# Kernel tuning notes

Measured on AMD Instinct MI355X. Metric: run time of the kernel, lower is better.

The kernel has to match this reference:

```python
import jax, jax.numpy as jnp
import numpy as np

N, E, R, B, H, C = 50000, 1600000, 50, 30, 16, 4


def setup_inputs() -> dict:
    key = jax.random.key(0)
    ks = jax.random.split(key, 12)
    edge_index = jax.random.randint(ks[0], (2, E), 0, N, dtype=jnp.int64)
    edge_type = jax.random.randint(ks[1], (E,), 0, R, dtype=jnp.int64)
    edge_norm = jax.random.uniform(ks[2], (E,), dtype=jnp.float32)
    s = 0.1
    basis1 = jax.random.normal(ks[3], (B, N, H), dtype=jnp.float32) * s
    comp1 = jax.random.normal(ks[4], (R, B), dtype=jnp.float32) * s
    root1 = jax.random.normal(ks[5], (N, H), dtype=jnp.float32) * s
    bias1 = jnp.zeros((H,), dtype=jnp.float32)
    basis2 = jax.random.normal(ks[6], (B, H, C), dtype=jnp.float32) * s
    comp2 = jax.random.normal(ks[7], (R, B), dtype=jnp.float32) * s
    root2 = jax.random.normal(ks[8], (H, C), dtype=jnp.float32) * s
    bias2 = jnp.zeros((C,), dtype=jnp.float32)
    return {
        "edge_index": edge_index, "edge_type": edge_type, "edge_norm": edge_norm,
        "basis1": basis1, "comp1": comp1, "root1": root1, "bias1": bias1,
        "basis2": basis2, "comp2": comp2, "root2": root2, "bias2": bias2,
    }


def _scatter_mean(msg, dst, n):
    # mean aggregation over destination nodes (PyG RGCNConv aggr='mean')
    summed = jnp.zeros((n, msg.shape[1]), dtype=msg.dtype).at[dst].add(msg)
    cnt = jnp.zeros((n,), dtype=msg.dtype).at[dst].add(1.0)
    return summed / jnp.maximum(cnt, 1.0)[:, None]


def reference(edge_index, edge_type, edge_norm, basis1, comp1, root1, bias1,
              basis2, comp2, root2, bias2):
    # edge_norm is accepted but unused, matching the original forward
    src, dst = edge_index[0], edge_index[1]
    n = root1.shape[0]
    # ---- layer 1: x is None -> per-(relation, src-node) weight row lookup ----
    w1 = jnp.einsum('rb,bnh->rnh', comp1, basis1)       # [R, N, H]
    msg1 = w1[edge_type, src]                           # [E, H] gather
    x = _scatter_mean(msg1, dst, n) + root1 + bias1      # root added directly (x=None)
    x = jax.nn.relu(x)
    # ---- layer 2: standard basis-decomposed RGCN on dense features ----
    w2 = jnp.einsum('rb,bhc->rhc', comp2, basis2)       # [R, H, C]
    msg2 = jnp.einsum('eh,ehc->ec', x[src], w2[edge_type])  # per-edge transform
    out = _scatter_mean(msg2, dst, n) + x @ root2 + bias2
    return jax.nn.log_softmax(out, axis=1)
```

## Files before the change

### kernel.cpp

```cpp
#include <hip/hip_runtime.h>
#include <math.h>

#define N_NODES 50000
#define E_EDGES 1600000
#define R_REL   50
#define B_BAS   30
#define H_DIM   16
#define C_DIM   4
#define NH      (N_NODES * H_DIM)

#define NSLICE      8
#define SLICE_NODES (N_NODES / NSLICE)

#define FRONT_BLOCKS (NH / 256)
#define EDGES_PER_FRONT (E_EDGES / FRONT_BLOCKS)

__global__ __launch_bounds__(256) void k_front(const float* __restrict__ basis1,
                                               const float* __restrict__ comp1,
                                               float* __restrict__ w1,
                                               const int* __restrict__ ei,
                                               int* __restrict__ cnt_i) {
    {
        const int ebase = blockIdx.x * EDGES_PER_FRONT + threadIdx.x;
        atomicAdd(&cnt_i[ei[E_EDGES + ebase]], 1);
        atomicAdd(&cnt_i[ei[E_EDGES + ebase + 256]], 1);
    }

    const int idx = blockIdx.x * 256 + threadIdx.x;
    float bv[B_BAS];
#pragma unroll
    for (int b = 0; b < B_BAS; ++b) bv[b] = basis1[b * NH + idx];

    for (int r = 0; r < R_REL; ++r) {
        float acc = 0.f;
#pragma unroll
        for (int b = 0; b < B_BAS; ++b) acc += comp1[r * B_BAS + b] * bv[b];
        w1[(size_t)r * NH + idx] = acc;
    }
}

__global__ __launch_bounds__(256) void k_scan_part(const int* __restrict__ cnt_i,
                                                   int* __restrict__ part,
                                                   int* __restrict__ bsum) {
    const int i = blockIdx.x * 256 + threadIdx.x;
    const int lane = threadIdx.x & 63;
    const int wid = threadIdx.x >> 6;
    const int v = (i < N_NODES) ? cnt_i[i] : 0;
    int s = v;
#pragma unroll
    for (int d = 1; d < 64; d <<= 1) {
        int t = __shfl_up(s, d, 64);
        if (lane >= d) s += t;
    }
    __shared__ int wsum[4];
    if (lane == 63) wsum[wid] = s;
    __syncthreads();
    int woff = 0;
    for (int w = 0; w < wid; ++w) woff += wsum[w];
    if (i < N_NODES) part[i] = s - v + woff;
    if (threadIdx.x == 255) bsum[blockIdx.x] = woff + s;
}

__global__ __launch_bounds__(256) void k_scan_tops(const int* __restrict__ bsum,
                                                   int* __restrict__ boff,
                                                   const float* __restrict__ basis2,
                                                   const float* __restrict__ comp2,
                                                   float* __restrict__ w2) {
    const int NB = (N_NODES + 255) / 256;
    const int lane = threadIdx.x & 63;
    const int wid = threadIdx.x >> 6;
    const int v = (threadIdx.x < NB) ? bsum[threadIdx.x] : 0;
    int s = v;
#pragma unroll
    for (int d = 1; d < 64; d <<= 1) {
        int t = __shfl_up(s, d, 64);
        if (lane >= d) s += t;
    }
    __shared__ int wsum[4];
    if (lane == 63) wsum[wid] = s;
    __syncthreads();
    int woff = 0;
    for (int w = 0; w < wid; ++w) woff += wsum[w];
    if (threadIdx.x < NB) boff[threadIdx.x] = s - v + woff;

    const int HC = H_DIM * C_DIM;
    for (int idx = threadIdx.x; idx < R_REL * HC; idx += 256) {
        const int r = idx / HC;
        const int hc = idx % HC;
        float acc = 0.f;
#pragma unroll
        for (int b = 0; b < B_BAS; ++b)
            acc += comp2[r * B_BAS + b] * basis2[b * HC + hc];
        w2[idx] = acc;
    }
}

__global__ __launch_bounds__(256) void k_scan_add(const int* __restrict__ part,
                                                  const int* __restrict__ boff,
                                                  int* __restrict__ off,
                                                  int* __restrict__ cursor) {
    const int i = blockIdx.x * 256 + threadIdx.x;
    if (i < N_NODES) {
        const int o = part[i] + boff[blockIdx.x];
        off[i] = o;
        cursor[i] = o;
    }
    if (i == 0) off[N_NODES] = E_EDGES;
}

__global__ __launch_bounds__(256) void k_bucket(const int* __restrict__ ei,
                                                const int* __restrict__ et,
                                                int* __restrict__ cursor,
                                                unsigned* __restrict__ rec) {
    const int chunk = blockIdx.x >> 3;
    const int slice = blockIdx.x & (NSLICE - 1);
    const int lo = slice * SLICE_NODES;

    const int e = chunk * 256 + threadIdx.x;
    if (e >= E_EDGES) return;
    const int dst = __builtin_nontemporal_load(&ei[E_EDGES + e]);
    if ((unsigned)(dst - lo) >= (unsigned)SLICE_NODES) return;

    const int src = __builtin_nontemporal_load(&ei[e]);
    const int r = __builtin_nontemporal_load(&et[e]);
    const int pos = atomicAdd(&cursor[dst], 1);
    rec[pos] = (unsigned)src | ((unsigned)r << 16);
}

__global__ __launch_bounds__(256) void k_agg1x(const unsigned* __restrict__ rec,
                                               const int* __restrict__ off,
                                               const float* __restrict__ w1,
                                               const float* __restrict__ root1,
                                               const float* __restrict__ bias1,
                                               float* __restrict__ x) {
    const int wid = threadIdx.x >> 6;
    const int lane = threadIdx.x & 63;
    const int dst = blockIdx.x * 4 + wid;
    const int h = lane & 15;
    const int sub = lane >> 4;
    const int e0 = off[dst], e1 = off[dst + 1];

    float acc = 0.f;
    for (int e = e0 + sub; e < e1; e += 4) {
        const unsigned p = rec[e];
        const int src = (int)(p & 0xFFFFu);
        const int r = (int)(p >> 16);
        acc += w1[(size_t)r * NH + src * H_DIM + h];
    }
    acc += __shfl_xor(acc, 16, 64);
    acc += __shfl_xor(acc, 32, 64);

    if (sub == 0) {
        const float c = fmaxf((float)(e1 - e0), 1.f);
        const float v = acc / c + root1[dst * H_DIM + h] + bias1[h];
        x[dst * H_DIM + h] = fmaxf(v, 0.f);
    }
}

__global__ __launch_bounds__(256) void k_agg2out(const unsigned* __restrict__ rec,
                                                 const int* __restrict__ off,
                                                 const float* __restrict__ x,
                                                 const float* __restrict__ w2,
                                                 const float* __restrict__ root2,
                                                 const float* __restrict__ bias2,
                                                 float* __restrict__ out) {
    const int wid = threadIdx.x >> 6;
    const int lane = threadIdx.x & 63;
    const int dst = blockIdx.x * 4 + wid;
    const int h = lane & 15;
    const int sub = lane >> 4;
    const int e0 = off[dst], e1 = off[dst + 1];

    float a0 = 0.f, a1 = 0.f, a2 = 0.f, a3 = 0.f;
    for (int e = e0 + sub; e < e1; e += 4) {
        const unsigned p = rec[e];
        const int src = (int)(p & 0xFFFFu);
        const int r = (int)(p >> 16);
        const float xv = x[src * H_DIM + h];
        const float4 w = *(const float4*)(w2 + r * (H_DIM * C_DIM) + h * C_DIM);
        a0 += xv * w.x; a1 += xv * w.y; a2 += xv * w.z; a3 += xv * w.w;
    }
#pragma unroll
    for (int d = 1; d < 64; d <<= 1) {
        a0 += __shfl_xor(a0, d, 64);
        a1 += __shfl_xor(a1, d, 64);
        a2 += __shfl_xor(a2, d, 64);
        a3 += __shfl_xor(a3, d, 64);
    }

    if (lane == 0) {
        const float c = fmaxf((float)(e1 - e0), 1.f);
        float y0 = a0 / c + bias2[0];
        float y1 = a1 / c + bias2[1];
        float y2 = a2 / c + bias2[2];
        float y3 = a3 / c + bias2[3];
#pragma unroll
        for (int hh = 0; hh < H_DIM; ++hh) {
            const float xv = x[dst * H_DIM + hh];
            const float4 w = *(const float4*)(root2 + hh * C_DIM);
            y0 += xv * w.x; y1 += xv * w.y; y2 += xv * w.z; y3 += xv * w.w;
        }
        const float m = fmaxf(fmaxf(y0, y1), fmaxf(y2, y3));
        const float s = expf(y0 - m) + expf(y1 - m) + expf(y2 - m) + expf(y3 - m);
        const float lse = m + logf(s);
        out[dst * 4 + 0] = y0 - lse;
        out[dst * 4 + 1] = y1 - lse;
        out[dst * 4 + 2] = y2 - lse;
        out[dst * 4 + 3] = y3 - lse;
    }
}

extern "C" void kernel_launch(void* const* d_in, const int* in_sizes, int n_in,
                              void* d_out, int out_size, void* d_ws, size_t ws_size,
                              hipStream_t stream) {
    const int*   edge_index = (const int*)d_in[0];
    const int*   edge_type  = (const int*)d_in[1];
    const float* basis1 = (const float*)d_in[3];
    const float* comp1  = (const float*)d_in[4];
    const float* root1  = (const float*)d_in[5];
    const float* bias1  = (const float*)d_in[6];
    const float* basis2 = (const float*)d_in[7];
    const float* comp2  = (const float*)d_in[8];
    const float* root2  = (const float*)d_in[9];
    const float* bias2  = (const float*)d_in[10];

    float* out = (float*)d_out;

    char* ws = (char*)d_ws;
    size_t o = 0;
    auto take = [&](size_t bytes) { char* p = ws + o; o += (bytes + 15) & ~(size_t)15; return p; };

    float*    w1     = (float*)   take((size_t)R_REL * NH * sizeof(float));
    unsigned* rec    = (unsigned*)take((size_t)E_EDGES * sizeof(unsigned));
    float*    x      = (float*)   take((size_t)NH * sizeof(float));
    int*      part   = (int*)x;
    int*      off    = (int*)     take((size_t)(N_NODES + 1) * sizeof(int));
    int*      cnt_i  = (int*)     take((size_t)N_NODES * sizeof(int));
    int*      cursor = (int*)     take((size_t)N_NODES * sizeof(int));
    float*    w2     = (float*)   take((size_t)R_REL * H_DIM * C_DIM * sizeof(float));
    int*      bsum   = (int*)     take(256 * sizeof(int));
    int*      boff   = (int*)     take(256 * sizeof(int));
    (void)ws_size;

    const int NB = (N_NODES + 255) / 256;

    hipMemsetAsync(cnt_i, 0, (size_t)N_NODES * sizeof(int), stream);

    k_front<<<FRONT_BLOCKS, 256, 0, stream>>>(basis1, comp1, w1, edge_index, cnt_i);

    k_scan_part<<<NB, 256, 0, stream>>>(cnt_i, part, bsum);
    k_scan_tops<<<1, 256, 0, stream>>>(bsum, boff, basis2, comp2, w2);
    k_scan_add<<<NB, 256, 0, stream>>>(part, boff, off, cursor);
    {
        const int chunks = (E_EDGES + 255) / 256;
        k_bucket<<<chunks * NSLICE, 256, 0, stream>>>(edge_index, edge_type, cursor, rec);
    }

    k_agg1x<<<N_NODES / 4, 256, 0, stream>>>(rec, off, w1, root1, bias1, x);

    k_agg2out<<<N_NODES / 4, 256, 0, stream>>>(rec, off, x, w2, root2, bias2, out);
}
```

Measured before the change: 426.9 us.

## Vectorize w1 basis combination with float4 and merge scan into single kernel

k_front now processes four w1 elements per thread with float4 loads and stores, which cuts the grid to 800 blocks, and counts the edges in those blocks with an 8-way unrolled loop. The three-kernel prefix scan (part, tops, add) is replaced by one 1024-thread single-block kernel in which each thread serially scans 49 contiguous counts and then does a wave/block scan. This removes two launches and the intermediate part/bsum arrays. The cost is that the scan runs on a single workgroup with strided, uncoalesced per-thread loads, and k_front uses more registers for 30 float4 basis values.

Result: slower. 545.0 us (+27.7%).

```diff
diff --git a/kernel.cpp b/kernel.cpp
--- a/kernel.cpp
+++ b/kernel.cpp
@@ -8,12 +8,13 @@
 #define H_DIM   16
 #define C_DIM   4
 #define NH      (N_NODES * H_DIM)
+#define NH4     (NH / 4)
 
 #define NSLICE      8
 #define SLICE_NODES (N_NODES / NSLICE)
 
-#define FRONT_BLOCKS (NH / 256)
-#define EDGES_PER_FRONT (E_EDGES / FRONT_BLOCKS)
+#define FRONT_BLOCKS    800
+#define EDGES_PER_BLOCK (E_EDGES / FRONT_BLOCKS)
 
 __global__ __launch_bounds__(256) void k_front(const float* __restrict__ basis1,
                                                const float* __restrict__ comp1,
@@ -21,70 +22,86 @@
                                                const int* __restrict__ ei,
                                                int* __restrict__ cnt_i) {
     {
-        const int ebase = blockIdx.x * EDGES_PER_FRONT + threadIdx.x;
-        atomicAdd(&cnt_i[ei[E_EDGES + ebase]], 1);
-        atomicAdd(&cnt_i[ei[E_EDGES + ebase + 256]], 1);
-    }
-
-    const int idx = blockIdx.x * 256 + threadIdx.x;
-    float bv[B_BAS];
-#pragma unroll
-    for (int b = 0; b < B_BAS; ++b) bv[b] = basis1[b * NH + idx];
+        const int ebase = blockIdx.x * EDGES_PER_BLOCK;
+#pragma unroll
+        for (int i = 0; i < 8; ++i) {
+            const int el = threadIdx.x + i * 256;
+            if (el < EDGES_PER_BLOCK)
+                atomicAdd(&cnt_i[ei[E_EDGES + ebase + el]], 1);
+        }
+    }
+
+    const int idx4 = blockIdx.x * 256 + threadIdx.x;
+    if (idx4 >= NH4) return;
+
+    float4 bv[B_BAS];
+#pragma unroll
+    for (int b = 0; b < B_BAS; ++b)
+        bv[b] = *(const float4*)(basis1 + (size_t)b * NH + idx4 * 4);
 
     for (int r = 0; r < R_REL; ++r) {
-        float acc = 0.f;
-#pragma unroll
-        for (int b = 0; b < B_BAS; ++b) acc += comp1[r * B_BAS + b] * bv[b];
-        w1[(size_t)r * NH + idx] = acc;
-    }
-}
-
-__global__ __launch_bounds__(256) void k_scan_part(const int* __restrict__ cnt_i,
-                                                   int* __restrict__ part,
-                                                   int* __restrict__ bsum) {
-    const int i = blockIdx.x * 256 + threadIdx.x;
-    const int lane = threadIdx.x & 63;
-    const int wid = threadIdx.x >> 6;
-    const int v = (i < N_NODES) ? cnt_i[i] : 0;
-    int s = v;
+        float4 acc = {0.f, 0.f, 0.f, 0.f};
+#pragma unroll
+        for (int b = 0; b < B_BAS; ++b) {
+            const float c = comp1[r * B_BAS + b];
+            acc.x += c * bv[b].x;
+            acc.y += c * bv[b].y;
+            acc.z += c * bv[b].z;
+            acc.w += c * bv[b].w;
+        }
+        *(float4*)(w1 + (size_t)r * NH + idx4 * 4) = acc;
+    }
+}
+
+#define SCAN_ITEMS 49
+
+__global__ __launch_bounds__(1024) void k_scan(const int* __restrict__ cnt_i,
+                                               int* __restrict__ off,
+                                               int* __restrict__ cursor,
+                                               const float* __restrict__ basis2,
+                                               const float* __restrict__ comp2,
+                                               float* __restrict__ w2) {
+    const int t = threadIdx.x;
+    const int lane = t & 63;
+    const int wid = t >> 6;
+    const int base = t * SCAN_ITEMS;
+
+    int loc[SCAN_ITEMS];
+    int sum = 0;
+#pragma unroll
+    for (int i = 0; i < SCAN_ITEMS; ++i) {
+        const int idx = base + i;
+        const int v = (idx < N_NODES) ? cnt_i[idx] : 0;
+        loc[i] = sum;
+        sum += v;
+    }
+
+    int s = sum;
 #pragma unroll
     for (int d = 1; d < 64; d <<= 1) {
-        int t = __shfl_up(s, d, 64);
-        if (lane >= d) s += t;
-    }
-    __shared__ int wsum[4];
+        const int tv = __shfl_up(s, d, 64);
+        if (lane >= d) s += tv;
+    }
+    __shared__ int wsum[16];
     if (lane == 63) wsum[wid] = s;
     __syncthreads();
     int woff = 0;
     for (int w = 0; w < wid; ++w) woff += wsum[w];
-    if (i < N_NODES) part[i] = s - v + woff;
-    if (threadIdx.x == 255) bsum[blockIdx.x] = woff + s;
-}
-
-__global__ __launch_bounds__(256) void k_scan_tops(const int* __restrict__ bsum,
-                                                   int* __restrict__ boff,
-                                                   const float* __restrict__ basis2,
-                                                   const float* __restrict__ comp2,
-                                                   float* __restrict__ w2) {
-    const int NB = (N_NODES + 255) / 256;
-    const int lane = threadIdx.x & 63;
-    const int wid = threadIdx.x >> 6;
-    const int v = (threadIdx.x < NB) ? bsum[threadIdx.x] : 0;
-    int s = v;
-#pragma unroll
-    for (int d = 1; d < 64; d <<= 1) {
-        int t = __shfl_up(s, d, 64);
-        if (lane >= d) s += t;
-    }
-    __shared__ int wsum[4];
-    if (lane == 63) wsum[wid] = s;
-    __syncthreads();
-    int woff = 0;
-    for (int w = 0; w < wid; ++w) woff += wsum[w];
-    if (threadIdx.x < NB) boff[threadIdx.x] = s - v + woff;
+    const int prefix = woff + s - sum;
+
+#pragma unroll
+    for (int i = 0; i < SCAN_ITEMS; ++i) {
+        const int idx = base + i;
+        if (idx < N_NODES) {
+            const int o = prefix + loc[i];
+            off[idx] = o;
+            cursor[idx] = o;
+        }
+    }
+    if (t == 0) off[N_NODES] = E_EDGES;
 
     const int HC = H_DIM * C_DIM;
-    for (int idx = threadIdx.x; idx < R_REL * HC; idx += 256) {
+    for (int idx = t; idx < R_REL * HC; idx += 1024) {
         const int r = idx / HC;
         const int hc = idx % HC;
         float acc = 0.f;
@@ -93,19 +110,6 @@
             acc += comp2[r * B_BAS + b] * basis2[b * HC + hc];
         w2[idx] = acc;
     }
-}
-
-__global__ __launch_bounds__(256) void k_scan_add(const int* __restrict__ part,
-                                                  const int* __restrict__ boff,
-                                                  int* __restrict__ off,
-                                                  int* __restrict__ cursor) {
-    const int i = blockIdx.x * 256 + threadIdx.x;
-    if (i < N_NODES) {
-        const int o = part[i] + boff[blockIdx.x];
-        off[i] = o;
-        cursor[i] = o;
-    }
-    if (i == 0) off[N_NODES] = E_EDGES;
 }
 
 __global__ __launch_bounds__(256) void k_bucket(const int* __restrict__ ei,
@@ -233,24 +237,18 @@
     float*    w1     = (float*)   take((size_t)R_REL * NH * sizeof(float));
     unsigned* rec    = (unsigned*)take((size_t)E_EDGES * sizeof(unsigned));
     float*    x      = (float*)   take((size_t)NH * sizeof(float));
-    int*      part   = (int*)x;
     int*      off    = (int*)     take((size_t)(N_NODES + 1) * sizeof(int));
     int*      cnt_i  = (int*)     take((size_t)N_NODES * sizeof(int));
     int*      cursor = (int*)     take((size_t)N_NODES * sizeof(int));
     float*    w2     = (float*)   take((size_t)R_REL * H_DIM * C_DIM * sizeof(float));
-    int*      bsum   = (int*)     take(256 * sizeof(int));
-    int*      boff   = (int*)     take(256 * sizeof(int));
     (void)ws_size;
 
-    const int NB = (N_NODES + 255) / 256;
-
     hipMemsetAsync(cnt_i, 0, (size_t)N_NODES * sizeof(int), stream);
 
     k_front<<<FRONT_BLOCKS, 256, 0, stream>>>(basis1, comp1, w1, edge_index, cnt_i);
 
-    k_scan_part<<<NB, 256, 0, stream>>>(cnt_i, part, bsum);
-    k_scan_tops<<<1, 256, 0, stream>>>(bsum, boff, basis2, comp2, w2);
-    k_scan_add<<<NB, 256, 0, stream>>>(part, boff, off, cursor);
+    k_scan<<<1, 1024, 0, stream>>>(cnt_i, off, cursor, basis2, comp2, w2);
+
     {
         const int chunks = (E_EDGES + 255) / 256;
         k_bucket<<<chunks * NSLICE, 256, 0, stream>>>(edge_index, edge_type, cursor, rec);
```
